# Kernel optimization log

Hardware: AMD Instinct MI355X
Metric: run time of the kernel (lower is better)

The kernel has to match this reference:

```python
import jax, jax.numpy as jnp
import numpy as np

DIVISOR = 2.0
NEGATIVE_SLOPE = 0.01


def setup_inputs() -> dict:
    key = jax.random.key(0)
    k1, k2, k3 = jax.random.split(key, 3)
    x = jax.random.normal(k1, (32, 128, 130, 130), dtype=jnp.float32)
    weight = jax.random.normal(k2, (256, 128, 3, 3), dtype=jnp.float32) * 0.05
    bias = jax.random.normal(k3, (256,), dtype=jnp.float32)
    return {"x": x, "weight": weight, "bias": bias}


def reference(x, weight, bias):
    # conv2d, stride=1, padding=0 (VALID), NCHW / OIHW layout
    y = jax.lax.conv_general_dilated(
        x, weight,
        window_strides=(1, 1),
        padding='VALID',
        dimension_numbers=('NCHW', 'OIHW', 'NCHW'),
    )
    y = y + bias[None, :, None, None]
    y = y * (1.0 / DIVISOR)
    # fused LeakyReLU epilogue
    return jnp.where(y >= 0, y, y * NEGATIVE_SLOPE)
```

## Files before the change

kernel.cpp:

```cpp
#include <hip/hip_runtime.h>
#include <hip/hip_bf16.h>
#include <stdint.h>

typedef __bf16 bf16x8 __attribute__((ext_vector_type(8)));
typedef float  f32x4  __attribute__((ext_vector_type(4)));
typedef unsigned short ushort8v __attribute__((ext_vector_type(8)));

#define NSLOPE 0.01f

#define NB   32
#define CIN  128
#define HIN  130
#define WIN  130
#define KOUT 256
#define POUT 128
#define QOUT 128
#define HWIN (HIN*WIN)
#define PQ   (POUT*QOUT)

#define XP_BYTES 138444800ull
#define WP_ELEMS (2*3*3*KOUT*64)

#define XT_OFF    16384
#define LDS_TOTAL (16384 + 16640)

__device__ __forceinline__ unsigned short f2bf(float f) {
    unsigned u = __builtin_bit_cast(unsigned, f);
    u += 0x7FFFu + ((u >> 16) & 1u);
    return (unsigned short)(u >> 16);
}

__device__ __forceinline__ void g2lds16(const void* g, void* l) {
    __builtin_amdgcn_global_load_lds(
        (const __attribute__((address_space(1))) void*)g,
        (__attribute__((address_space(3))) void*)l,
        16, 0, 0);
}

__global__ __launch_bounds__(256) void k_conv_x(const float* __restrict__ X,
                                                unsigned short* __restrict__ Xp) {
    __shared__ unsigned short tile[130*132];
    const int b = blockIdx.x;
    const int n = b / 130, h = b - n*130;
    const int tid = threadIdx.x;
    const size_t in_base = (size_t)n*(CIN*(size_t)HWIN) + (size_t)h*WIN;
    for (int fi = tid; fi < CIN*65; fi += 256) {
        int c = fi / 65, w2 = fi - c*65;
        float2 v = *(const float2*)(X + in_base + (size_t)c*HWIN + w2*2);
        tile[(w2*2  )*132 + c] = f2bf(v.x);
        tile[(w2*2+1)*132 + c] = f2bf(v.y);
    }
    __syncthreads();
    unsigned short* outp = Xp + (size_t)b * (WIN*CIN);
    for (int oi = tid; oi < (WIN*CIN)/8; oi += 256) {
        int e = oi*8; int w = e >> 7; int c8 = e & 127;
        const unsigned short* t = &tile[w*132 + c8];
        ushort8v v;
        #pragma unroll
        for (int j = 0; j < 8; ++j) v[j] = t[j];
        *(ushort8v*)(outp + e) = v;
    }
}

__global__ __launch_bounds__(256) void k_conv_w(const float* __restrict__ W,
                                                unsigned short* __restrict__ Wp) {
    int e = blockIdx.x*256 + threadIdx.x;
    if (e >= WP_ELEMS) return;
    int ci = e & 63;
    int k  = (e >> 6) & 255;
    int rsIdx = e >> 14;
    int cc = rsIdx / 9; int rem = rsIdx - cc*9; int r = rem / 3, s = rem - r*3;
    int c = cc*64 + ci;
    Wp[e] = f2bf(W[(size_t)k*1152 + (size_t)c*9 + r*3 + s]);
}

__global__ __launch_bounds__(128, 2) void k_conv_main(
    const unsigned short* __restrict__ Xp,
    const unsigned short* __restrict__ Wp,
    const float* __restrict__ bias,
    float* __restrict__ out)
{
    __shared__ __align__(16) unsigned char smem[LDS_TOTAL];

    const int tid  = threadIdx.x;
    const int lane = tid & 63;
    const int wm   = tid >> 6;
    const int l15  = lane & 15;
    const int kg16 = (lane >> 4) << 4;

    const int L  = ((blockIdx.x & 7) << 10) | (blockIdx.x >> 3);
    const int kh = L & 1;
    const int np = L >> 1;
    const int p  = np & 127;
    const int n  = np >> 7;

    f32x4 acc[4][8];
    #pragma unroll
    for (int i = 0; i < 4; ++i)
        #pragma unroll
        for (int j = 0; j < 8; ++j)
            acc[i][j] = (f32x4){0.f, 0.f, 0.f, 0.f};

    #pragma unroll 1
    for (int t = 0; t < 18; ++t) {
        const int cc = t / 9;
        const int rem = t - cc*9;
        const int r  = rem / 3;
        const int s  = rem - r*3;

        __syncthreads();

        {
            const unsigned short* wbase = Wp + (size_t)t*(KOUT*64) + (size_t)(kh*128)*64;
            #pragma unroll
            for (int it = 0; it < 8; ++it) {
                const int g    = it*128 + tid;
                const int phys = g << 4;
                const int row  = phys >> 7;
                const int cib  = (phys & 127) ^ ((row & 7) << 4);
                g2lds16(wbase + (size_t)row*64 + (cib >> 1), smem + phys);
            }
        }
        if (s == 0) {
            const unsigned short* xbase =
                Xp + ((size_t)((n*HIN + (p + r))*WIN))*CIN + cc*64;
            #pragma unroll
            for (int it = 0; it < 9; ++it) {
                const int g = it*128 + tid;
                if (g < 1040) {
                    const int phys = g << 4;
                    const int w    = phys >> 7;
                    const int cib  = (phys & 127) ^ ((w & 7) << 4);
                    g2lds16(xbase + (size_t)w*CIN + (cib >> 1), smem + XT_OFF + phys);
                }
            }
        }

        __syncthreads();

        #pragma unroll
        for (int kq = 0; kq < 2; ++kq) {
            const int cib0 = kq*64 + kg16;
            bf16x8 A[4], B[8];
            #pragma unroll
            for (int mf = 0; mf < 4; ++mf) {
                const int row = wm*64 + mf*16 + l15;
                A[mf] = *(const bf16x8*)(smem + row*128 + (cib0 ^ ((row & 7) << 4)));
            }
            #pragma unroll
            for (int nf = 0; nf < 8; ++nf) {
                const int g = nf*16 + l15 + s;
                B[nf] = *(const bf16x8*)(smem + XT_OFF + g*128 + (cib0 ^ ((g & 7) << 4)));
            }
            #pragma unroll
            for (int mf = 0; mf < 4; ++mf)
                #pragma unroll
                for (int nf = 0; nf < 8; ++nf)
                    acc[mf][nf] = __builtin_amdgcn_mfma_f32_16x16x32_bf16(
                        A[mf], B[nf], acc[mf][nf], 0, 0, 0);
        }
    }

    const int kg = lane >> 4;
    #pragma unroll
    for (int mf = 0; mf < 4; ++mf) {
        const int kb = kh*128 + wm*64 + mf*16 + kg*4;
        const float4 bv = *(const float4*)(bias + kb);
        const float bj[4] = {bv.x, bv.y, bv.z, bv.w};
        #pragma unroll
        for (int nf = 0; nf < 8; ++nf) {
            const int q = nf*16 + l15;
            const size_t base = (((size_t)n*KOUT + kb)*POUT + p)*QOUT + q;
            #pragma unroll
            for (int j = 0; j < 4; ++j) {
                float y = (acc[mf][nf][j] + bj[j]) * 0.5f;
                out[base + (size_t)j*PQ] = (y >= 0.f) ? y : y*NSLOPE;
            }
        }
    }
}

extern "C" void kernel_launch(void* const* d_in, const int* in_sizes, int n_in,
                              void* d_out, int out_size, void* d_ws, size_t ws_size,
                              hipStream_t stream) {
    const float* X = (const float*)d_in[0];
    const float* W = (const float*)d_in[1];
    const float* B = (const float*)d_in[2];
    float* out = (float*)d_out;
    unsigned short* Xp = (unsigned short*)d_ws;
    unsigned short* Wp = (unsigned short*)((char*)d_ws + XP_BYTES);

    k_conv_x   <<<NB*HIN, 256, 0, stream>>>(X, Xp);
    k_conv_w   <<<(WP_ELEMS + 255)/256, 256, 0, stream>>>(W, Wp);
    k_conv_main<<<8192, 128, 0, stream>>>(Xp, Wp, B, out);
}
```

Before: 425.7 us.

## Load weights directly from global in MFMA fragment order, cut LDS syncs

```diff
diff --git a/kernel.cpp b/kernel.cpp
--- a/kernel.cpp
+++ b/kernel.cpp
@@ -19,10 +19,9 @@
 #define PQ   (POUT*QOUT)
 
 #define XP_BYTES 138444800ull
-#define WP_ELEMS (2*3*3*KOUT*64)
+#define WP_ELEMS (18*2*8*2*64*8)
 
-#define XT_OFF    16384
-#define LDS_TOTAL (16384 + 16640)
+#define LDS_TOTAL 16640
 
 __device__ __forceinline__ unsigned short f2bf(float f) {
     unsigned u = __builtin_bit_cast(unsigned, f);
@@ -66,33 +65,40 @@
                                                 unsigned short* __restrict__ Wp) {
     int e = blockIdx.x*256 + threadIdx.x;
     if (e >= WP_ELEMS) return;
-    int ci = e & 63;
-    int k  = (e >> 6) & 255;
-    int rsIdx = e >> 14;
-    int cc = rsIdx / 9; int rem = rsIdx - cc*9; int r = rem / 3, s = rem - r*3;
-    int c = cc*64 + ci;
-    Wp[e] = f2bf(W[(size_t)k*1152 + (size_t)c*9 + r*3 + s]);
+    int j     = e & 7;
+    int lane  = (e >> 3) & 63;
+    int kq    = (e >> 9) & 1;
+    int fr    = (e >> 10) & 7;
+    int kh    = (e >> 13) & 1;
+    int rsidx = e >> 14;
+    int cc = rsidx / 9; int rem = rsidx - cc*9; int rr = rem / 3, s = rem - rr*3;
+    int kout = kh*128 + fr*16 + (lane & 15);
+    int ci   = cc*64 + kq*32 + (lane >> 4)*8 + j;
+    Wp[e] = f2bf(W[(size_t)kout*1152 + (size_t)ci*9 + rr*3 + s]);
 }
 
 __global__ __launch_bounds__(128, 2) void k_conv_main(
     const unsigned short* __restrict__ Xp,
-    const unsigned short* __restrict__ Wp,
+    const unsigned short* __restrict__ Wpp,
     const float* __restrict__ bias,
     float* __restrict__ out)
 {
-    __shared__ __align__(16) unsigned char smem[LDS_TOTAL];
+    __shared__ __align__(16) unsigned char xs[LDS_TOTAL];
 
     const int tid  = threadIdx.x;
     const int lane = tid & 63;
     const int wm   = tid >> 6;
     const int l15  = lane & 15;
     const int kg16 = (lane >> 4) << 4;
+    const int laneB = lane << 4;
 
     const int L  = ((blockIdx.x & 7) << 10) | (blockIdx.x >> 3);
     const int kh = L & 1;
     const int np = L >> 1;
     const int p  = np & 127;
     const int n  = np >> 7;
+
+    const unsigned char* wfp = (const unsigned char*)Wpp + (kh << 14) + (wm << 13) + laneB;
 
     f32x4 acc[4][8];
     #pragma unroll
@@ -102,26 +108,12 @@
             acc[i][j] = (f32x4){0.f, 0.f, 0.f, 0.f};
 
     #pragma unroll 1
-    for (int t = 0; t < 18; ++t) {
-        const int cc = t / 9;
-        const int rem = t - cc*9;
-        const int r  = rem / 3;
-        const int s  = rem - r*3;
+    for (int cr = 0; cr < 6; ++cr) {
+        const int cc = cr / 3;
+        const int r  = cr - cc*3;
 
         __syncthreads();
-
         {
-            const unsigned short* wbase = Wp + (size_t)t*(KOUT*64) + (size_t)(kh*128)*64;
-            #pragma unroll
-            for (int it = 0; it < 8; ++it) {
-                const int g    = it*128 + tid;
-                const int phys = g << 4;
-                const int row  = phys >> 7;
-                const int cib  = (phys & 127) ^ ((row & 7) << 4);
-                g2lds16(wbase + (size_t)row*64 + (cib >> 1), smem + phys);
-            }
-        }
-        if (s == 0) {
             const unsigned short* xbase =
                 Xp + ((size_t)((n*HIN + (p + r))*WIN))*CIN + cc*64;
             #pragma unroll
@@ -131,33 +123,34 @@
                     const int phys = g << 4;
                     const int w    = phys >> 7;
                     const int cib  = (phys & 127) ^ ((w & 7) << 4);
-                    g2lds16(xbase + (size_t)w*CIN + (cib >> 1), smem + XT_OFF + phys);
+                    g2lds16(xbase + (size_t)w*CIN + (cib >> 1), xs + phys);
                 }
             }
         }
-
         __syncthreads();
 
         #pragma unroll
-        for (int kq = 0; kq < 2; ++kq) {
-            const int cib0 = kq*64 + kg16;
-            bf16x8 A[4], B[8];
+        for (int s = 0; s < 3; ++s) {
+            const unsigned char* wb = wfp + (size_t)(cr*3 + s)*32768;
             #pragma unroll
-            for (int mf = 0; mf < 4; ++mf) {
-                const int row = wm*64 + mf*16 + l15;
-                A[mf] = *(const bf16x8*)(smem + row*128 + (cib0 ^ ((row & 7) << 4)));
+            for (int kq = 0; kq < 2; ++kq) {
+                bf16x8 A[4], B[8];
+                #pragma unroll
+                for (int mf = 0; mf < 4; ++mf)
+                    A[mf] = *(const bf16x8*)(wb + kq*1024 + mf*2048);
+                const int cib0 = kq*64 + kg16;
+                #pragma unroll
+                for (int nf = 0; nf < 8; ++nf) {
+                    const int g = nf*16 + l15 + s;
+                    B[nf] = *(const bf16x8*)(xs + g*128 + (cib0 ^ ((g & 7) << 4)));
+                }
+                #pragma unroll
+                for (int mf = 0; mf < 4; ++mf)
+                    #pragma unroll
+                    for (int nf = 0; nf < 8; ++nf)
+                        acc[mf][nf] = __builtin_amdgcn_mfma_f32_16x16x32_bf16(
+                            A[mf], B[nf], acc[mf][nf], 0, 0, 0);
             }
-            #pragma unroll
-            for (int nf = 0; nf < 8; ++nf) {
-                const int g = nf*16 + l15 + s;
-                B[nf] = *(const bf16x8*)(smem + XT_OFF + g*128 + (cib0 ^ ((g & 7) << 4)));
-            }
-            #pragma unroll
-            for (int mf = 0; mf < 4; ++mf)
-                #pragma unroll
-                for (int nf = 0; nf < 8; ++nf)
-                    acc[mf][nf] = __builtin_amdgcn_mfma_f32_16x16x32_bf16(
-                        A[mf], B[nf], acc[mf][nf], 0, 0, 0);
         }
     }
 
```

New measurement: 575.3 us. +35.2%, slower.

## Enlarge conv tile to 256 channels by two output rows with double-buffered weights

Applied to the files above, without the earlier changes.

```diff
diff --git a/kernel.cpp b/kernel.cpp
--- a/kernel.cpp
+++ b/kernel.cpp
@@ -21,8 +21,9 @@
 #define XP_BYTES 138444800ull
 #define WP_ELEMS (2*3*3*KOUT*64)
 
-#define XT_OFF    16384
-#define LDS_TOTAL (16384 + 16640)
+#define WS_BYTES 32768
+#define XS_BASE  65536
+#define LDS_TOTAL 132096
 
 __device__ __forceinline__ unsigned short f2bf(float f) {
     unsigned u = __builtin_bit_cast(unsigned, f);
@@ -74,103 +75,128 @@
     Wp[e] = f2bf(W[(size_t)k*1152 + (size_t)c*9 + r*3 + s]);
 }
 
-__global__ __launch_bounds__(128, 2) void k_conv_main(
+__device__ __forceinline__ void stage_w(const unsigned short* __restrict__ Wp,
+                                        unsigned char* lds, int rsidx, int tid) {
+    const unsigned short* wbase = Wp + (size_t)rsidx * (KOUT*64);
+    #pragma unroll
+    for (int it = 0; it < 8; ++it) {
+        const int t    = it*256 + tid;
+        const int phys = t << 4;
+        const int row  = phys >> 7;
+        const int cib  = (phys & 127) ^ ((row & 7) << 4);
+        g2lds16(wbase + (size_t)row*64 + (cib >> 1), lds + phys);
+    }
+}
+
+__device__ __forceinline__ void stage_x4(const unsigned short* __restrict__ Xp,
+                                         unsigned char* lds, int n, int p2, int cc, int tid) {
+    #pragma unroll
+    for (int it = 0; it < 17; ++it) {
+        const int t = it*256 + tid;
+        if (t < 4160) {
+            const int phys = t << 4;
+            const int g    = phys >> 7;
+            const int rloc = g / 130;
+            const int w    = g - 130*rloc;
+            const int cib  = (phys & 127) ^ ((g & 7) << 4);
+            const unsigned short* src =
+                Xp + ((size_t)((n*HIN + p2 + rloc)*WIN + w))*CIN + cc*64 + (cib >> 1);
+            g2lds16(src, lds + phys);
+        }
+    }
+}
+
+__global__ __launch_bounds__(256, 1) void k_conv_main(
     const unsigned short* __restrict__ Xp,
     const unsigned short* __restrict__ Wp,
     const float* __restrict__ bias,
     float* __restrict__ out)
 {
-    __shared__ __align__(16) unsigned char smem[LDS_TOTAL];
+    extern __shared__ __align__(16) unsigned char smem[];
 
     const int tid  = threadIdx.x;
     const int lane = tid & 63;
-    const int wm   = tid >> 6;
+    const int wid  = tid >> 6;
+    const int wmw  = wid >> 1;
+    const int wnw  = wid & 1;
     const int l15  = lane & 15;
     const int kg16 = (lane >> 4) << 4;
 
-    const int L  = ((blockIdx.x & 7) << 10) | (blockIdx.x >> 3);
-    const int kh = L & 1;
-    const int np = L >> 1;
-    const int p  = np & 127;
-    const int n  = np >> 7;
-
-    f32x4 acc[4][8];
-    #pragma unroll
-    for (int i = 0; i < 4; ++i)
+    const int L  = ((blockIdx.x & 7) << 8) | (blockIdx.x >> 3);
+    const int n  = L >> 6;
+    const int p2 = (L & 63) << 1;
+
+    unsigned char* xs = smem + XS_BASE;
+
+    const int rowA0 = wmw*128 + l15;
+    const int swA   = (l15 & 7) << 4;
+
+    f32x4 acc[8][8];
+    #pragma unroll
+    for (int i = 0; i < 8; ++i)
         #pragma unroll
         for (int j = 0; j < 8; ++j)
             acc[i][j] = (f32x4){0.f, 0.f, 0.f, 0.f};
 
+    stage_w(Wp, smem, 0, tid);
+    stage_x4(Xp, xs, n, p2, 0, tid);
+    asm volatile("s_waitcnt vmcnt(0)" ::: "memory");
+    __syncthreads();
+
     #pragma unroll 1
     for (int t = 0; t < 18; ++t) {
-        const int cc = t / 9;
+        const int cc  = t / 9;
         const int rem = t - cc*9;
-        const int r  = rem / 3;
-        const int s  = rem - r*3;
-
-        __syncthreads();
-
-        {
-            const unsigned short* wbase = Wp + (size_t)t*(KOUT*64) + (size_t)(kh*128)*64;
-            #pragma unroll
-            for (int it = 0; it < 8; ++it) {
-                const int g    = it*128 + tid;
-                const int phys = g << 4;
-                const int row  = phys >> 7;
-                const int cib  = (phys & 127) ^ ((row & 7) << 4);
-                g2lds16(wbase + (size_t)row*64 + (cib >> 1), smem + phys);
-            }
-        }
-        if (s == 0) {
-            const unsigned short* xbase =
-                Xp + ((size_t)((n*HIN + (p + r))*WIN))*CIN + cc*64;
-            #pragma unroll
-            for (int it = 0; it < 9; ++it) {
-                const int g = it*128 + tid;
-                if (g < 1040) {
-                    const int phys = g << 4;
-                    const int w    = phys >> 7;
-                    const int cib  = (phys & 127) ^ ((w & 7) << 4);
-                    g2lds16(xbase + (size_t)w*CIN + (cib >> 1), smem + XT_OFF + phys);
-                }
-            }
-        }
-
-        __syncthreads();
+        const int rr  = rem / 3;
+        const int s   = rem - rr*3;
+        unsigned char* wsR = smem + (t & 1)*WS_BYTES;
+        unsigned char* wsW = smem + ((t + 1) & 1)*WS_BYTES;
+
+        if (t < 17) stage_w(Wp, wsW, t + 1, tid);
+
+        const int g0  = (wnw + rr)*130 + l15 + s;
+        const int swB = (g0 & 7) << 4;
 
         #pragma unroll
         for (int kq = 0; kq < 2; ++kq) {
             const int cib0 = kq*64 + kg16;
-            bf16x8 A[4], B[8];
-            #pragma unroll
-            for (int mf = 0; mf < 4; ++mf) {
-                const int row = wm*64 + mf*16 + l15;
-                A[mf] = *(const bf16x8*)(smem + row*128 + (cib0 ^ ((row & 7) << 4)));
-            }
-            #pragma unroll
-            for (int nf = 0; nf < 8; ++nf) {
-                const int g = nf*16 + l15 + s;
-                B[nf] = *(const bf16x8*)(smem + XT_OFF + g*128 + (cib0 ^ ((g & 7) << 4)));
-            }
-            #pragma unroll
-            for (int mf = 0; mf < 4; ++mf)
+            const int aB = rowA0*128 + (cib0 ^ swA);
+            const int bB = g0*128   + (cib0 ^ swB);
+            bf16x8 A[8], B[8];
+            #pragma unroll
+            for (int mf = 0; mf < 8; ++mf)
+                A[mf] = *(const bf16x8*)(wsR + aB + mf*2048);
+            #pragma unroll
+            for (int nf = 0; nf < 8; ++nf)
+                B[nf] = *(const bf16x8*)(xs + bB + nf*2048);
+            #pragma unroll
+            for (int mf = 0; mf < 8; ++mf)
                 #pragma unroll
                 for (int nf = 0; nf < 8; ++nf)
                     acc[mf][nf] = __builtin_amdgcn_mfma_f32_16x16x32_bf16(
                         A[mf], B[nf], acc[mf][nf], 0, 0, 0);
         }
+
+        asm volatile("s_waitcnt vmcnt(0)" ::: "memory");
+        __syncthreads();
+
+        if (t == 8) {
+            stage_x4(Xp, xs, n, p2, 1, tid);
+            asm volatile("s_waitcnt vmcnt(0)" ::: "memory");
+            __syncthreads();
+        }
     }
 
     const int kg = lane >> 4;
     #pragma unroll
-    for (int mf = 0; mf < 4; ++mf) {
-        const int kb = kh*128 + wm*64 + mf*16 + kg*4;
+    for (int mf = 0; mf < 8; ++mf) {
+        const int kb = wmw*128 + mf*16 + kg*4;
         const float4 bv = *(const float4*)(bias + kb);
         const float bj[4] = {bv.x, bv.y, bv.z, bv.w};
         #pragma unroll
         for (int nf = 0; nf < 8; ++nf) {
             const int q = nf*16 + l15;
-            const size_t base = (((size_t)n*KOUT + kb)*POUT + p)*QOUT + q;
+            const size_t base = (((size_t)n*KOUT + kb)*POUT + (p2 + wnw))*QOUT + q;
             #pragma unroll
             for (int j = 0; j < 4; ++j) {
                 float y = (acc[mf][nf][j] + bj[j]) * 0.5f;
@@ -190,7 +216,10 @@
     unsigned short* Xp = (unsigned short*)d_ws;
     unsigned short* Wp = (unsigned short*)((char*)d_ws + XP_BYTES);
 
+    (void)hipFuncSetAttribute((const void*)k_conv_main,
+                              hipFuncAttributeMaxDynamicSharedMemorySize, LDS_TOTAL);
+
     k_conv_x   <<<NB*HIN, 256, 0, stream>>>(X, Xp);
     k_conv_w   <<<(WP_ELEMS + 255)/256, 256, 0, stream>>>(W, Wp);
-    k_conv_main<<<8192, 128, 0, stream>>>(Xp, Wp, B, out);
-}
+    k_conv_main<<<2048, 256, LDS_TOTAL, stream>>>(Xp, Wp, B, out);
+}
```

Result: slower. 813.3 us (+91.1%).
